# Optimization experiments

Measured on AMD Instinct MI355X. Metric: run time of the kernel, lower is better.

Reference implementation:

```python
import math
import jax, jax.numpy as jnp
import numpy as np

B, S, D_IN = 2, 2048, 1024
DKQ, DV, H = 1024, 1024, 16
HEAD_SIZE = DKQ / H  # attention_head_size (float division, as in torch)


def setup_inputs() -> dict:
    key = jax.random.key(0)
    k1, k2, k3, k4, k5, k6 = jax.random.split(key, 6)
    std = 1.0 / math.sqrt(D_IN)
    return {
        'hidden_states': jax.random.normal(k1, (B, S, D_IN), dtype=jnp.float32),
        'Wq': jax.random.normal(k2, (DKQ, D_IN), dtype=jnp.float32) * std,
        'Wk': jax.random.normal(k3, (DKQ, D_IN), dtype=jnp.float32) * std,
        'Wv': jax.random.normal(k4, (DV, D_IN), dtype=jnp.float32) * std,
        'bv': jax.random.normal(k5, (DV,), dtype=jnp.float32) * std,
        'mixing': jax.random.normal(k6, (H, DKQ), dtype=jnp.float32) * 0.2,  # UNIFORM init: normal(std=0.2)
    }


def reference(hidden_states, Wq, Wk, Wv, bv, mixing):
    # Q, K: [B, S, DKQ]; V: [B, S, DV]
    q = jnp.einsum('bsd,ed->bse', hidden_states, Wq)
    k = jnp.einsum('bsd,ed->bse', hidden_states, Wk)
    v = jnp.einsum('bsd,ed->bse', hidden_states, Wv) + bv
    # per-head query mixing: mixed_q[b,h,s,e] = q[b,s,e] * mixing[h,e]
    # scores[b,h,s,t] = sum_e mixed_q[b,h,s,e] * k[b,t,e]
    scores = jnp.einsum('bse,he,bte->bhst', q, mixing, k)
    scores = scores / math.sqrt(HEAD_SIZE)
    probs = jax.nn.softmax(scores, axis=-1)
    # value heads: [B, H, S, DV/H]
    v_h = v.reshape(v.shape[0], v.shape[1], H, DV // H).transpose(0, 2, 1, 3)
    ctx = jnp.einsum('bhst,bhtd->bhsd', probs, v_h)
    # back to [B, S, DV]
    ctx = ctx.transpose(0, 2, 1, 3).reshape(hidden_states.shape[0], hidden_states.shape[1], DV)
    return ctx
```

## Files before the change

### kernel.cpp

```cpp
#include <hip/hip_runtime.h>

#define B_ 2
#define S_ 2048
#define D_ 1024
#define H_ 16
#define HD_ 64

typedef _Float16 f16;
typedef _Float16 half8 __attribute__((ext_vector_type(8)));
typedef float float4_ __attribute__((ext_vector_type(4)));

#define N_HS (B_*S_*D_)
#define N_W  (D_*D_)
#define N_MIX (H_*D_)

__device__ __forceinline__ void gl_lds16(const f16* g, const f16* l) {
  __builtin_amdgcn_global_load_lds(
      (const __attribute__((address_space(1))) void*)g,
      (__attribute__((address_space(3))) void*)l, 16, 0, 0);
}

#define MIX_SCALE 0.18033688011112042f

__global__ __launch_bounds__(256) void convert_kernel(
    const float* __restrict__ hs, const float* __restrict__ wq,
    const float* __restrict__ wk, const float* __restrict__ wv,
    const float* __restrict__ mix,
    f16* __restrict__ hs16, f16* __restrict__ wq16, f16* __restrict__ wk16,
    f16* __restrict__ wv16, f16* __restrict__ mix16)
{
  const int total4 = (N_HS + 3*N_W + N_MIX) / 4;
  for (int i4 = blockIdx.x*blockDim.x + threadIdx.x; i4 < total4;
       i4 += gridDim.x*blockDim.x) {
    int i = i4*4;
    const float* src; f16* dst; float scale = 1.0f; int off;
    if (i < N_HS)            { src=hs;  dst=hs16;  off=i; }
    else if (i < N_HS+N_W)   { src=wq;  dst=wq16;  off=i-N_HS; }
    else if (i < N_HS+2*N_W) { src=wk;  dst=wk16;  off=i-N_HS-N_W; }
    else if (i < N_HS+3*N_W) { src=wv;  dst=wv16;  off=i-N_HS-2*N_W; }
    else                     { src=mix; dst=mix16; off=i-N_HS-3*N_W; scale=MIX_SCALE; }
    float4 v = *(const float4*)(src+off);
    dst[off]   = (f16)(v.x*scale);
    dst[off+1] = (f16)(v.y*scale);
    dst[off+2] = (f16)(v.z*scale);
    dst[off+3] = (f16)(v.w*scale);
  }
}

#define BM 128
#define BN 128
#define BK 64
#define LDA 72

__global__ __launch_bounds__(256, 2) void qkv_kernel(
    const f16* __restrict__ hs16, const f16* __restrict__ w16base,
    const float* __restrict__ bv,
    f16* __restrict__ q16, f16* __restrict__ k16, f16* __restrict__ vT)
{
  const int z = blockIdx.z;
  const f16* W = w16base + (size_t)z * N_W;
  f16* out = (z==0) ? q16 : k16;
  const int mt = blockIdx.y, nt = blockIdx.x;
  const int tid = threadIdx.x;
  const int lane = tid & 63, wid = tid >> 6;
  const int wm = wid >> 1, wn = wid & 1;
  const int quad = lane >> 4, l16 = lane & 15;

  __shared__ __align__(16) f16 As[BM*BK];
  __shared__ __align__(16) f16 Bs[BN*BK];

  float4_ acc[4][4];
#pragma unroll
  for (int i=0;i<4;i++)
#pragma unroll
    for (int j=0;j<4;j++) acc[i][j] = (float4_)0.0f;

  const int row0 = mt*BM;
  const int col0 = nt*BN;

  for (int ko = 0; ko < D_; ko += BK) {
#pragma unroll
    for (int c=0; c<4; c++) {
      int slot = (wid*4+c)*64 + lane;
      int r = slot >> 3;
      int gc = (slot & 7) ^ (r & 7);
      gl_lds16(hs16 + (size_t)(row0+r)*D_ + ko + gc*8, As + (size_t)(wid*4+c)*64*8);
      gl_lds16(W    + (size_t)(col0+r)*D_ + ko + gc*8, Bs + (size_t)(wid*4+c)*64*8);
    }
    __syncthreads();
#pragma unroll
    for (int kk=0; kk<BK; kk+=32) {
      int ck = (kk >> 3) + quad;
      half8 a[4], b[4];
#pragma unroll
      for (int i=0;i<4;i++) {
        int rr = wm*64 + i*16 + l16;
        a[i] = *(const half8*)&As[(size_t)(((rr<<3) | (ck ^ (rr&7))) << 3)];
      }
#pragma unroll
      for (int j=0;j<4;j++) {
        int rr = wn*64 + j*16 + l16;
        b[j] = *(const half8*)&Bs[(size_t)(((rr<<3) | (ck ^ (rr&7))) << 3)];
      }
#pragma unroll
      for (int i=0;i<4;i++)
#pragma unroll
        for (int j=0;j<4;j++)
          acc[i][j] = __builtin_amdgcn_mfma_f32_16x16x32_f16(a[i], b[j], acc[i][j], 0,0,0);
    }
    __syncthreads();
  }
#pragma unroll
  for (int i=0;i<4;i++) {
#pragma unroll
    for (int j=0;j<4;j++) {
      int colg = col0 + wn*64 + j*16 + l16;
      float bias = (z==2) ? bv[colg] : 0.0f;
#pragma unroll
      for (int r=0;r<4;r++) {
        int rowg = row0 + wm*64 + i*16 + quad*4 + r;
        f16 val = (f16)(acc[i][j][r] + bias);
        if (z == 2) {
          int bb = rowg >> 11, ss = rowg & (S_-1);
          vT[((size_t)bb*D_ + colg)*S_ + ss] = val;
        } else {
          out[(size_t)rowg*D_ + colg] = val;
        }
      }
    }
  }
}

#define TQ 128
#define TK 128
#define LDP 136

__global__ __launch_bounds__(256, 2) void attn_kernel(
    const f16* __restrict__ q16, const f16* __restrict__ k16,
    const f16* __restrict__ vT, const f16* __restrict__ mix16,
    float* __restrict__ out)
{
  const int b = blockIdx.z;
  const int h = blockIdx.y;
  const int s0 = blockIdx.x * TQ;
  const int tid = threadIdx.x;
  const int lane = tid & 63, wid = tid >> 6;
  const int wm = wid >> 1, wn = wid & 1;
  const int quad = lane >> 4, l16 = lane & 15;

  __shared__ __align__(16) union {
    struct { f16 q[TQ][LDA]; f16 k0[TK*BK]; f16 k1[TK*BK]; } s1;
    f16 P[TQ][LDP];
  } u;
  __shared__ __align__(16) float red_l[2][TQ];

  float l_lane[16];
#pragma unroll
  for (int t=0;t<16;t++) l_lane[t] = 0.0f;

  float4_ o_acc[4][2];
#pragma unroll
  for (int i=0;i<4;i++)
#pragma unroll
    for (int j=0;j<2;j++) o_acc[i][j] = (float4_)0.0f;

  const f16* qbase = q16 + (size_t)(b*S_ + s0)*D_;
  const f16* kbase = k16 + (size_t)b*S_*D_;
  const f16* mrow  = mix16 + h*D_;
  const f16* vTb   = vT + (size_t)(b*D_ + h*HD_)*S_;

  for (int t0 = 0; t0 < S_; t0 += 2*TK) {
    float4_ sacc[2][4][4];
#pragma unroll
    for (int tt=0;tt<2;tt++)
#pragma unroll
      for (int i=0;i<4;i++)
#pragma unroll
        for (int j=0;j<4;j++) sacc[tt][i][j] = (float4_)0.0f;

    for (int ko = 0; ko < D_; ko += BK) {
      const f16* k0g = kbase + (size_t)t0*D_ + ko;
      const f16* k1g = k0g + (size_t)TK*D_;
#pragma unroll
      for (int c=0; c<4; c++) {
        int slot = (wid*4+c)*64 + lane;
        int r = slot >> 3;
        int gc = (slot & 7) ^ (r & 7);
        gl_lds16(k0g + (size_t)r*D_ + gc*8, u.s1.k0 + (size_t)(wid*4+c)*64*8);
        gl_lds16(k1g + (size_t)r*D_ + gc*8, u.s1.k1 + (size_t)(wid*4+c)*64*8);
      }
#pragma unroll
      for (int it=0; it<4; it++) {
        int c = it*256 + tid;
        int r = c >> 3, c8 = (c & 7)*8;
        half8 qv = *(const half8*)&qbase[(size_t)r*D_ + ko + c8];
        half8 mv = *(const half8*)&mrow[ko + c8];
        *(half8*)&u.s1.q[r][c8] = qv * mv;
      }
      __syncthreads();
#pragma unroll
      for (int kk=0; kk<BK; kk+=32) {
        half8 a[4];
#pragma unroll
        for (int i=0;i<4;i++) a[i] = *(const half8*)&u.s1.q[wm*64+i*16+l16][kk+quad*8];
#pragma unroll
        for (int tt=0;tt<2;tt++) {
          const f16* kb = tt ? u.s1.k1 : u.s1.k0;
          half8 bf[4];
#pragma unroll
          for (int j=0;j<4;j++) {
            int rr = wn*64 + j*16 + l16;
            int ck = (kk >> 3) + quad;
            bf[j] = *(const half8*)&kb[(size_t)(((rr<<3) | (ck ^ (rr&7))) << 3)];
          }
#pragma unroll
          for (int i=0;i<4;i++)
#pragma unroll
            for (int j=0;j<4;j++)
              sacc[tt][i][j] = __builtin_amdgcn_mfma_f32_16x16x32_f16(a[i], bf[j], sacc[tt][i][j], 0,0,0);
        }
      }
      __syncthreads();
    }

#pragma unroll
    for (int tt=0;tt<2;tt++) {
#pragma unroll
      for (int i=0;i<4;i++)
#pragma unroll
        for (int j=0;j<4;j++)
#pragma unroll
          for (int r=0;r<4;r++) {
            float p = __builtin_exp2f(sacc[tt][i][j][r]);
            l_lane[i*4+r] += p;
            u.P[wm*64+i*16+quad*4+r][wn*64+j*16+l16] = (f16)p;
          }

      half8 vb[8];
#pragma unroll
      for (int ki=0; ki<4; ki++)
#pragma unroll
        for (int j=0; j<2; j++) {
          int ch = wn*32 + j*16 + l16;
          vb[ki*2+j] = *(const half8*)&vTb[(size_t)ch*S_ + t0 + tt*TK + ki*32 + quad*8];
        }

      __syncthreads();

#pragma unroll
      for (int ki=0; ki<4; ki++) {
        half8 pa[4];
#pragma unroll
        for (int i=0;i<4;i++) pa[i] = *(const half8*)&u.P[wm*64+i*16+l16][ki*32+quad*8];
#pragma unroll
        for (int i=0;i<4;i++)
#pragma unroll
          for (int j=0;j<2;j++)
            o_acc[i][j] = __builtin_amdgcn_mfma_f32_16x16x32_f16(pa[i], vb[ki*2+j], o_acc[i][j], 0,0,0);
      }
      __syncthreads();
    }
  }

#pragma unroll
  for (int d=1; d<16; d<<=1)
#pragma unroll
    for (int t=0;t<16;t++) l_lane[t] += __shfl_xor(l_lane[t], d);
  if (l16 == 0) {
#pragma unroll
    for (int i=0;i<4;i++)
#pragma unroll
      for (int r=0;r<4;r++)
        red_l[wn][wm*64+i*16+quad*4+r] = l_lane[i*4+r];
  }
  __syncthreads();

#pragma unroll
  for (int i=0;i<4;i++) {
#pragma unroll
    for (int r=0;r<4;r++) {
      int row = wm*64 + i*16 + quad*4 + r;
      float linv = 1.0f / (red_l[0][row] + red_l[1][row]);
#pragma unroll
      for (int j=0;j<2;j++) {
        int colg = h*HD_ + wn*32 + j*16 + l16;
        out[(size_t)(b*S_ + s0 + row)*D_ + colg] = o_acc[i][j][r] * linv;
      }
    }
  }
}

extern "C" void kernel_launch(void* const* d_in, const int* in_sizes, int n_in,
                              void* d_out, int out_size, void* d_ws, size_t ws_size,
                              hipStream_t stream) {
  (void)in_sizes; (void)n_in; (void)out_size; (void)ws_size;
  const float* hs  = (const float*)d_in[0];
  const float* Wq  = (const float*)d_in[1];
  const float* Wk  = (const float*)d_in[2];
  const float* Wv  = (const float*)d_in[3];
  const float* bv  = (const float*)d_in[4];
  const float* mix = (const float*)d_in[5];
  float* out = (float*)d_out;

  char* ws = (char*)d_ws;
  f16* hs16  = (f16*)(ws);
  f16* w16   = (f16*)(ws + 8388608);
  f16* mix16 = (f16*)(ws + 14680064);
  f16* q16   = (f16*)(ws + 14712832);
  f16* k16   = (f16*)(ws + 23101440);
  f16* vT    = (f16*)(ws + 31490048);

  convert_kernel<<<2048, 256, 0, stream>>>(hs, Wq, Wk, Wv, mix,
                                           hs16, w16, w16+N_W, w16+2*N_W, mix16);
  qkv_kernel<<<dim3(D_/BN, (B_*S_)/BM, 3), 256, 0, stream>>>(
      hs16, w16, bv, q16, k16, vT);
  attn_kernel<<<dim3(S_/TQ, H_, B_), 256, 0, stream>>>(
      q16, k16, vT, mix16, out);
}
```

Before: 469.8 us.

## Double-buffer K tiles in attention, load mixed Q directly into registers

Measured after the change: 856.7 us. +82.3%, slower.

```diff
diff --git a/kernel.cpp b/kernel.cpp
--- a/kernel.cpp
+++ b/kernel.cpp
@@ -50,7 +50,6 @@
 #define BM 128
 #define BN 128
 #define BK 64
-#define LDA 72
 
 __global__ __launch_bounds__(256, 2) void qkv_kernel(
     const f16* __restrict__ hs16, const f16* __restrict__ w16base,
@@ -149,7 +148,7 @@
   const int quad = lane >> 4, l16 = lane & 15;
 
   __shared__ __align__(16) union {
-    struct { f16 q[TQ][LDA]; f16 k0[TK*BK]; f16 k1[TK*BK]; } s1;
+    f16 k[4][TK*BK];
     f16 P[TQ][LDP];
   } u;
   __shared__ __align__(16) float red_l[2][TQ];
@@ -169,6 +168,20 @@
   const f16* mrow  = mix16 + h*D_;
   const f16* vTb   = vT + (size_t)(b*D_ + h*HD_)*S_;
 
+#define STAGE_PAIR(p, t0g, ko_) do {                                         \
+    const f16* k0g_ = kbase + (size_t)(t0g)*D_ + (ko_);                      \
+    const f16* k1g_ = k0g_ + (size_t)TK*D_;                                  \
+    _Pragma("unroll")                                                        \
+    for (int c_=0; c_<4; c_++) {                                             \
+      int slot_ = (wid*4+c_)*64 + lane;                                      \
+      int r_ = slot_ >> 3;                                                   \
+      int gc_ = (slot_ & 7) ^ (r_ & 7);                                      \
+      gl_lds16(k0g_ + (size_t)r_*D_ + gc_*8, u.k[2*(p)]   + (size_t)(wid*4+c_)*64*8); \
+      gl_lds16(k1g_ + (size_t)r_*D_ + gc_*8, u.k[2*(p)+1] + (size_t)(wid*4+c_)*64*8); \
+    } } while (0)
+
+  STAGE_PAIR(0, 0, 0);
+
   for (int t0 = 0; t0 < S_; t0 += 2*TK) {
     float4_ sacc[2][4][4];
 #pragma unroll
@@ -178,39 +191,30 @@
 #pragma unroll
         for (int j=0;j<4;j++) sacc[tt][i][j] = (float4_)0.0f;
 
-    for (int ko = 0; ko < D_; ko += BK) {
-      const f16* k0g = kbase + (size_t)t0*D_ + ko;
-      const f16* k1g = k0g + (size_t)TK*D_;
-#pragma unroll
-      for (int c=0; c<4; c++) {
-        int slot = (wid*4+c)*64 + lane;
-        int r = slot >> 3;
-        int gc = (slot & 7) ^ (r & 7);
-        gl_lds16(k0g + (size_t)r*D_ + gc*8, u.s1.k0 + (size_t)(wid*4+c)*64*8);
-        gl_lds16(k1g + (size_t)r*D_ + gc*8, u.s1.k1 + (size_t)(wid*4+c)*64*8);
-      }
-#pragma unroll
-      for (int it=0; it<4; it++) {
-        int c = it*256 + tid;
-        int r = c >> 3, c8 = (c & 7)*8;
-        half8 qv = *(const half8*)&qbase[(size_t)r*D_ + ko + c8];
-        half8 mv = *(const half8*)&mrow[ko + c8];
-        *(half8*)&u.s1.q[r][c8] = qv * mv;
-      }
+#pragma unroll 2
+    for (int ko_i = 0; ko_i < D_/BK; ko_i++) {
+      const int ko = ko_i * BK;
+      const int cur = ko_i & 1;
       __syncthreads();
-#pragma unroll
-      for (int kk=0; kk<BK; kk+=32) {
+      if (ko_i < D_/BK - 1) STAGE_PAIR(cur^1, t0, ko + BK);
+
+      __builtin_amdgcn_s_setprio(1);
+#pragma unroll
+      for (int kk2=0; kk2<2; kk2++) {
+        const int kc = ko + kk2*32 + quad*8;
+        half8 mv = *(const half8*)&mrow[kc];
         half8 a[4];
 #pragma unroll
-        for (int i=0;i<4;i++) a[i] = *(const half8*)&u.s1.q[wm*64+i*16+l16][kk+quad*8];
+        for (int i=0;i<4;i++)
+          a[i] = *(const half8*)&qbase[(size_t)(wm*64 + i*16 + l16)*D_ + kc] * mv;
 #pragma unroll
         for (int tt=0;tt<2;tt++) {
-          const f16* kb = tt ? u.s1.k1 : u.s1.k0;
+          const f16* kb = u.k[2*cur + tt];
           half8 bf[4];
 #pragma unroll
           for (int j=0;j<4;j++) {
             int rr = wn*64 + j*16 + l16;
-            int ck = (kk >> 3) + quad;
+            int ck = kk2*4 + quad;
             bf[j] = *(const half8*)&kb[(size_t)(((rr<<3) | (ck ^ (rr&7))) << 3)];
           }
 #pragma unroll
@@ -220,8 +224,9 @@
               sacc[tt][i][j] = __builtin_amdgcn_mfma_f32_16x16x32_f16(a[i], bf[j], sacc[tt][i][j], 0,0,0);
         }
       }
-      __syncthreads();
-    }
+      __builtin_amdgcn_s_setprio(0);
+    }
+    __syncthreads();
 
 #pragma unroll
     for (int tt=0;tt<2;tt++) {
@@ -247,6 +252,7 @@
 
       __syncthreads();
 
+      __builtin_amdgcn_s_setprio(1);
 #pragma unroll
       for (int ki=0; ki<4; ki++) {
         half8 pa[4];
@@ -258,8 +264,11 @@
           for (int j=0;j<2;j++)
             o_acc[i][j] = __builtin_amdgcn_mfma_f32_16x16x32_f16(pa[i], vb[ki*2+j], o_acc[i][j], 0,0,0);
       }
+      __builtin_amdgcn_s_setprio(0);
       __syncthreads();
     }
+
+    if (t0 + 2*TK < S_) STAGE_PAIR(0, t0 + 2*TK, 0);
   }
 
 #pragma unroll
```
